# Optimization experiments

Measured on AMD Instinct MI355X. Metric: run time of the kernel, lower is better.

The kernel has to match this reference:

```python
import jax, jax.numpy as jnp
import numpy as np
from jax import lax

B, H, W = 512, 128, 128
ARCH = [1, 4096, 4096, 4096, 4096]
CONV_THRESH = 0.0
GRAPH_THRESH = 0.8
EMBED_DIM = 1


def setup_inputs() -> dict:
    key = jax.random.key(0)
    ks = jax.random.split(key, 16)
    inp = {
        "x": jax.random.normal(ks[0], (B, 1, H, W), dtype=jnp.float32),
        "conv_w": jax.random.normal(ks[1], (1, 1, 2, 2), dtype=jnp.float32) * 0.5,
        "conv_b": jax.random.normal(ks[2], (1,), dtype=jnp.float32) * 0.1,
        "rotation": jax.random.normal(ks[3], (EMBED_DIM, EMBED_DIM), dtype=jnp.float32),
        "entangle": jax.random.normal(ks[4], (EMBED_DIM, EMBED_DIM), dtype=jnp.float32),
    }
    # Linear params, torch convention W: [out_f, in_f]
    for i, (fi, fo) in enumerate(zip(ARCH[:-1], ARCH[1:])):
        inp[f"W{i+1}"] = jax.random.normal(ks[5 + 2 * i], (fo, fi), dtype=jnp.float32) / np.sqrt(fi)
        inp[f"b{i+1}"] = jax.random.normal(ks[6 + 2 * i], (fo,), dtype=jnp.float32) * 0.01
    return inp


def _forward(x, conv_w, conv_b, rotation, entangle, W1, b1, W2, b2, W3, b3, W4, b4):
    # ConvFilter: 2x2 valid conv, sigmoid(logits - thresh), mean over C,H,W -> [B]
    logits = lax.conv_general_dilated(
        x, conv_w, window_strides=(1, 1), padding="VALID",
        dimension_numbers=("NCHW", "OIHW", "NCHW"))
    logits = logits + conv_b.reshape(1, -1, 1, 1)
    conv_out = jax.nn.sigmoid(logits - CONV_THRESH).mean(axis=(1, 2, 3))  # [B]
    conv_vec = conv_out[:, None]  # [B, 1] -> embed_dim forced to 1

    # ClassicalSelfAttention (embed_dim = 1)
    q = conv_vec @ rotation                      # [B, 1]
    k = conv_vec @ entangle                      # [B, 1]
    scores = jax.nn.softmax((q @ k.T) / np.sqrt(EMBED_DIM).astype(np.float32), axis=-1)  # [B, B]
    attn_out = scores @ conv_vec                 # [B, 1]

    # tanh MLP stack
    out = attn_out
    acts = []
    for Wl, bl in ((W1, b1), (W2, b2), (W3, b3), (W4, b4)):
        out = jnp.tanh(out @ Wl.T + bl)          # [B, out_f]
        acts.append(out)

    # Vectorized fidelity adjacency over equal-shaped layer activations:
    # normalized Gram matrix squared, thresholded (replaces the O(L^2)
    # Python loop with .item() syncs in the source).
    S = jnp.stack([a.reshape(-1) for a in acts])                  # [L, B*4096]
    S_hat = S / (jnp.linalg.norm(S, axis=1, keepdims=True) + 1e-12)
    fid = (S_hat @ S_hat.T) ** 2                                   # [L, L]
    L = len(acts)
    weights = jnp.where(fid >= GRAPH_THRESH, 1.0, 0.0) * (1.0 - jnp.eye(L, dtype=fid.dtype))
    return out, weights


def reference(x, conv_w, conv_b, rotation, entangle, W1, b1, W2, b2, W3, b3, W4, b4):
    return _forward(x, conv_w, conv_b, rotation, entangle, W1, b1, W2, b2, W3, b3, W4, b4)
```

## Files before the change

### kernel.cpp

```cpp
#include <hip/hip_runtime.h>
#include <cmath>


#define NEL (512 * 4096)

typedef float  floatx4 __attribute__((ext_vector_type(4)));
typedef _Float16 halfx8 __attribute__((ext_vector_type(8)));

__global__ __launch_bounds__(256) void conv_mean_kernel(
    const float* __restrict__ x, const float* __restrict__ cw,
    const float* __restrict__ cb, float* __restrict__ c_out)
{
  __shared__ float sbuf[4];
  const int b = blockIdx.x;
  const float w00 = cw[0], w01 = cw[1], w10 = cw[2], w11 = cw[3];
  const float bias = cb[0];
  const float* xb = x + (size_t)b * 128 * 128;
  float acc = 0.f;
  for (int idx = threadIdx.x; idx < 127 * 127; idx += 256) {
    int i = idx / 127;
    int j = idx - i * 127;
    const float* p = xb + i * 128 + j;
    float v = w00 * p[0] + w01 * p[1] + w10 * p[128] + w11 * p[129] + bias;
    acc += 1.0f / (1.0f + __expf(-v));
  }
  #pragma unroll
  for (int off = 32; off > 0; off >>= 1) acc += __shfl_down(acc, off, 64);
  const int lane = threadIdx.x & 63, wv = threadIdx.x >> 6;
  if (lane == 0) sbuf[wv] = acc;
  __syncthreads();
  if (threadIdx.x == 0)
    c_out[b] = (sbuf[0] + sbuf[1] + sbuf[2] + sbuf[3]) * (1.0f / 16129.0f);
}

__global__ __launch_bounds__(64) void attn_kernel(
    const float* __restrict__ c, const float* __restrict__ rot,
    const float* __restrict__ ent, float* __restrict__ attn)
{
  const int i = blockIdx.x;
  const int lane = threadIdx.x;
  const float t = rot[0] * ent[0] * c[i];
  float vals[8], cj[8];
  float mx = -1e30f;
  #pragma unroll
  for (int u = 0; u < 8; ++u) {
    float cv = c[lane + u * 64];
    cj[u] = cv;
    vals[u] = t * cv;
    mx = fmaxf(mx, vals[u]);
  }
  #pragma unroll
  for (int off = 32; off > 0; off >>= 1) mx = fmaxf(mx, __shfl_down(mx, off, 64));
  mx = __shfl(mx, 0, 64);
  float se = 0.f, sw = 0.f;
  #pragma unroll
  for (int u = 0; u < 8; ++u) {
    float e = __expf(vals[u] - mx);
    se += e;
    sw += e * cj[u];
  }
  #pragma unroll
  for (int off = 32; off > 0; off >>= 1) {
    se += __shfl_down(se, off, 64);
    sw += __shfl_down(sw, off, 64);
  }
  if (lane == 0) attn[i] = sw / se;
}

__global__ __launch_bounds__(256) void layer1_kernel(
    const float* __restrict__ attn, const float* __restrict__ W1,
    const float* __restrict__ b1, float* __restrict__ act1)
{
  const int o = blockIdx.x * 256 + threadIdx.x;
  const int i = blockIdx.y;
  act1[(size_t)i * 4096 + o] = tanhf(attn[i] * W1[o] + b1[o]);
}

#define BM 128
#define BN 128
#define BK 32
#define LDK 40

template<bool FUSE>
__global__ __launch_bounds__(256) void gemm_tanh_kernel(
    const float* __restrict__ A, const float* __restrict__ W,
    const float* __restrict__ bias, float* __restrict__ C)
{
  __shared__ _Float16 As[BM][LDK];
  __shared__ _Float16 Ws[BN][LDK];
  const int K = 4096, N = 4096;
  const int tid  = threadIdx.x;
  const int lane = tid & 63;
  const int wave = tid >> 6;
  const int wm = (wave >> 1) * 64;
  const int wn = (wave & 1) * 64;
  const int q  = lane >> 4;
  const int ml = lane & 15;
  const int tileM = blockIdx.y * BM;
  const int tileN = blockIdx.x * BN;
  const int Kslice = K / gridDim.z;
  const int kbeg = blockIdx.z * Kslice;
  const int kend = kbeg + Kslice;
  float* Cb = FUSE ? C : C + (size_t)blockIdx.z * NEL;

  floatx4 acc[4][4] = {};

  const int r0  = tid >> 2;
  const int cc0 = (tid & 3) << 3;

  float4 pa[4], pw[4];
  auto load_tile = [&](int k0) {
    #pragma unroll
    for (int u = 0; u < 2; ++u) {
      const float* ap = A + (size_t)(tileM + r0 + u * 64) * K + k0 + cc0;
      pa[2 * u]     = *reinterpret_cast<const float4*>(ap);
      pa[2 * u + 1] = *reinterpret_cast<const float4*>(ap + 4);
      const float* wp = W + (size_t)(tileN + r0 + u * 64) * K + k0 + cc0;
      pw[2 * u]     = *reinterpret_cast<const float4*>(wp);
      pw[2 * u + 1] = *reinterpret_cast<const float4*>(wp + 4);
    }
  };
  auto store_tile = [&]() {
    #pragma unroll
    for (int u = 0; u < 2; ++u) {
      halfx8 ha = { (_Float16)pa[2*u].x, (_Float16)pa[2*u].y,
                    (_Float16)pa[2*u].z, (_Float16)pa[2*u].w,
                    (_Float16)pa[2*u+1].x, (_Float16)pa[2*u+1].y,
                    (_Float16)pa[2*u+1].z, (_Float16)pa[2*u+1].w };
      *reinterpret_cast<halfx8*>(&As[r0 + u * 64][cc0]) = ha;
      halfx8 hw = { (_Float16)pw[2*u].x, (_Float16)pw[2*u].y,
                    (_Float16)pw[2*u].z, (_Float16)pw[2*u].w,
                    (_Float16)pw[2*u+1].x, (_Float16)pw[2*u+1].y,
                    (_Float16)pw[2*u+1].z, (_Float16)pw[2*u+1].w };
      *reinterpret_cast<halfx8*>(&Ws[r0 + u * 64][cc0]) = hw;
    }
  };

  load_tile(kbeg);
  for (int k0 = kbeg; k0 < kend; k0 += BK) {
    __syncthreads();
    store_tile();
    __syncthreads();
    if (k0 + BK < kend) load_tile(k0 + BK);

    halfx8 af[4], bf[4];
    #pragma unroll
    for (int i = 0; i < 4; ++i)
      af[i] = *reinterpret_cast<const halfx8*>(&As[wm + i * 16 + ml][q * 8]);
    #pragma unroll
    for (int j = 0; j < 4; ++j)
      bf[j] = *reinterpret_cast<const halfx8*>(&Ws[wn + j * 16 + ml][q * 8]);

    #pragma unroll
    for (int i = 0; i < 4; ++i)
      #pragma unroll
      for (int j = 0; j < 4; ++j)
        acc[i][j] = __builtin_amdgcn_mfma_f32_16x16x32_f16(af[i], bf[j], acc[i][j], 0, 0, 0);
  }

  #pragma unroll
  for (int i = 0; i < 4; ++i) {
    const int row0 = tileM + wm + i * 16 + q * 4;
    #pragma unroll
    for (int j = 0; j < 4; ++j) {
      const int col = tileN + wn + j * 16 + ml;
      if (FUSE) {
        const float bv = bias[col];
        #pragma unroll
        for (int r = 0; r < 4; ++r)
          Cb[(size_t)(row0 + r) * N + col] = tanhf(acc[i][j][r] + bv);
      } else {
        #pragma unroll
        for (int r = 0; r < 4; ++r)
          Cb[(size_t)(row0 + r) * N + col] = acc[i][j][r];
      }
    }
  }
}

template<int S>
__global__ __launch_bounds__(256) void combine_tanh_kernel(
    const float* __restrict__ part, const float* __restrict__ bias,
    float* __restrict__ outp)
{
  const int i4 = blockIdx.x * 256 + threadIdx.x;
  const floatx4* p4 = (const floatx4*)part;
  floatx4 s = p4[i4];
  #pragma unroll
  for (int z = 1; z < S; ++z) s += p4[(size_t)z * (NEL / 4) + i4];
  const floatx4 bv = ((const floatx4*)bias)[i4 & 1023];
  floatx4 o;
  #pragma unroll
  for (int r = 0; r < 4; ++r) o[r] = tanhf(s[r] + bv[r]);
  ((floatx4*)outp)[i4] = o;
}

__global__ __launch_bounds__(256) void fid_dots_kernel(
    const float* __restrict__ a1, const float* __restrict__ a2,
    const float* __restrict__ a3, const float* __restrict__ a4,
    float* __restrict__ D)
{
  __shared__ float sred[4][10];
  float s[10] = {0, 0, 0, 0, 0, 0, 0, 0, 0, 0};
  const int n4 = NEL / 4;
  const int stride = gridDim.x * blockDim.x;
  const floatx4* p1 = (const floatx4*)a1;
  const floatx4* p2 = (const floatx4*)a2;
  const floatx4* p3 = (const floatx4*)a3;
  const floatx4* p4 = (const floatx4*)a4;
  for (int i = blockIdx.x * 256 + threadIdx.x; i < n4; i += stride) {
    floatx4 v1 = p1[i], v2 = p2[i], v3 = p3[i], v4 = p4[i];
    #pragma unroll
    for (int r = 0; r < 4; ++r) {
      s[0] += v1[r] * v1[r]; s[1] += v1[r] * v2[r]; s[2] += v1[r] * v3[r];
      s[3] += v1[r] * v4[r]; s[4] += v2[r] * v2[r]; s[5] += v2[r] * v3[r];
      s[6] += v2[r] * v4[r]; s[7] += v3[r] * v3[r]; s[8] += v3[r] * v4[r];
      s[9] += v4[r] * v4[r];
    }
  }
  const int lane = threadIdx.x & 63, wv = threadIdx.x >> 6;
  #pragma unroll
  for (int p = 0; p < 10; ++p) {
    float v = s[p];
    #pragma unroll
    for (int off = 32; off > 0; off >>= 1) v += __shfl_down(v, off, 64);
    if (lane == 0) sred[wv][p] = v;
  }
  __syncthreads();
  if (threadIdx.x < 10) {
    float v = sred[0][threadIdx.x] + sred[1][threadIdx.x] +
              sred[2][threadIdx.x] + sred[3][threadIdx.x];
    atomicAdd(&D[threadIdx.x * 16], v);
  }
}

__global__ void finalize_kernel(const float* __restrict__ D, float* __restrict__ wout)
{
  const int i = threadIdx.x;
  if (i >= 16) return;
  const int p = i >> 2, qq = i & 3;
  const int a = p < qq ? p : qq;
  const int b = p < qq ? qq : p;
  const int base[4] = {0, 4, 7, 9};
  const float dpq = D[(base[a] + (b - a)) * 16];
  const float npv = sqrtf(D[base[p] * 16]) + 1e-12f;
  const float nqv = sqrtf(D[base[qq] * 16]) + 1e-12f;
  const float ch = dpq / (npv * nqv);
  const float fid = ch * ch;
  wout[i] = (fid >= 0.8f && p != qq) ? 1.0f : 0.0f;
}

extern "C" void kernel_launch(void* const* d_in, const int* in_sizes, int n_in,
                              void* d_out, int out_size, void* d_ws, size_t ws_size,
                              hipStream_t stream)
{
  const float* x   = (const float*)d_in[0];
  const float* cw  = (const float*)d_in[1];
  const float* cb  = (const float*)d_in[2];
  const float* rot = (const float*)d_in[3];
  const float* ent = (const float*)d_in[4];
  const float* W1  = (const float*)d_in[5];
  const float* b1  = (const float*)d_in[6];
  const float* W2  = (const float*)d_in[7];
  const float* b2  = (const float*)d_in[8];
  const float* W3  = (const float*)d_in[9];
  const float* b3  = (const float*)d_in[10];
  const float* W4  = (const float*)d_in[11];
  const float* b4  = (const float*)d_in[12];
  float* out = (float*)d_out;

  char*  ws    = (char*)d_ws;
  float* c_buf = (float*)(ws + 0);
  float* attn  = (float*)(ws + 2048);
  float* D     = (float*)(ws + 4096);
  float* act1  = (float*)(ws + 8192);
  float* act2  = act1 + NEL;
  float* act3  = act2 + NEL;
  float* part  = act3 + NEL;
  float* wout  = out + NEL;

  const size_t base_need = 8192 + (size_t)3 * NEL * 4;
  const bool sk8 = ws_size >= base_need + (size_t)8 * NEL * 4;
  const bool sk4 = ws_size >= base_need + (size_t)4 * NEL * 4;

  hipMemsetAsync(D, 0, 10 * 16 * sizeof(float), stream);
  conv_mean_kernel<<<512, 256, 0, stream>>>(x, cw, cb, c_buf);
  attn_kernel<<<512, 64, 0, stream>>>(c_buf, rot, ent, attn);
  layer1_kernel<<<dim3(16, 512), 256, 0, stream>>>(attn, W1, b1, act1);

  const int cgrid = NEL / 4 / 256;
  if (sk8) {
    dim3 g(4096 / BN, 512 / BM, 8);
    gemm_tanh_kernel<false><<<g, 256, 0, stream>>>(act1, W2, nullptr, part);
    combine_tanh_kernel<8><<<cgrid, 256, 0, stream>>>(part, b2, act2);
    gemm_tanh_kernel<false><<<g, 256, 0, stream>>>(act2, W3, nullptr, part);
    combine_tanh_kernel<8><<<cgrid, 256, 0, stream>>>(part, b3, act3);
    gemm_tanh_kernel<false><<<g, 256, 0, stream>>>(act3, W4, nullptr, part);
    combine_tanh_kernel<8><<<cgrid, 256, 0, stream>>>(part, b4, out);
  } else if (sk4) {
    dim3 g(4096 / BN, 512 / BM, 4);
    gemm_tanh_kernel<false><<<g, 256, 0, stream>>>(act1, W2, nullptr, part);
    combine_tanh_kernel<4><<<cgrid, 256, 0, stream>>>(part, b2, act2);
    gemm_tanh_kernel<false><<<g, 256, 0, stream>>>(act2, W3, nullptr, part);
    combine_tanh_kernel<4><<<cgrid, 256, 0, stream>>>(part, b3, act3);
    gemm_tanh_kernel<false><<<g, 256, 0, stream>>>(act3, W4, nullptr, part);
    combine_tanh_kernel<4><<<cgrid, 256, 0, stream>>>(part, b4, out);
  } else {
    dim3 g(4096 / BN, 512 / BM, 1);
    gemm_tanh_kernel<true><<<g, 256, 0, stream>>>(act1, W2, b2, act2);
    gemm_tanh_kernel<true><<<g, 256, 0, stream>>>(act2, W3, b3, act3);
    gemm_tanh_kernel<true><<<g, 256, 0, stream>>>(act3, W4, b4, out);
  }

  fid_dots_kernel<<<256, 256, 0, stream>>>(act1, act2, act3, out, D);
  finalize_kernel<<<1, 64, 0, stream>>>(D, wout);
}
```

Before: 456.2 us.

## Double-buffer GEMM LDS tiles and vectorize conv loads

The GEMM kernel now uses two LDS buffers, so the next tile is written into the idle buffer after the MFMAs. This cuts the loop to one barrier per K step and lets the global loads overlap the matrix math. Launch bounds now request 4 blocks per SIMD, which may raise register pressure or cause spills. The conv kernel now reads each row with float4 loads and computes four outputs per thread instead of indexing each output with a division.

```diff
diff --git a/kernel.cpp b/kernel.cpp
--- a/kernel.cpp
+++ b/kernel.cpp
@@ -17,12 +17,24 @@
   const float bias = cb[0];
   const float* xb = x + (size_t)b * 128 * 128;
   float acc = 0.f;
-  for (int idx = threadIdx.x; idx < 127 * 127; idx += 256) {
-    int i = idx / 127;
-    int j = idx - i * 127;
-    const float* p = xb + i * 128 + j;
-    float v = w00 * p[0] + w01 * p[1] + w10 * p[128] + w11 * p[129] + bias;
-    acc += 1.0f / (1.0f + __expf(-v));
+  for (int t = threadIdx.x; t < 127 * 32; t += 256) {
+    const int i  = t >> 5;
+    const int j0 = (t & 31) << 2;
+    const float* pr0 = xb + i * 128 + j0;
+    const float* pr1 = pr0 + 128;
+    const float4 a4 = *reinterpret_cast<const float4*>(pr0);
+    const float  a5 = pr0[4];
+    const float4 b4 = *reinterpret_cast<const float4*>(pr1);
+    const float  b5 = pr1[4];
+    const float a[5] = {a4.x, a4.y, a4.z, a4.w, a5};
+    const float bb[5] = {b4.x, b4.y, b4.z, b4.w, b5};
+    #pragma unroll
+    for (int m = 0; m < 4; ++m) {
+      if (j0 + m < 127) {
+        float v = w00 * a[m] + w01 * a[m + 1] + w10 * bb[m] + w11 * bb[m + 1] + bias;
+        acc += 1.0f / (1.0f + __expf(-v));
+      }
+    }
   }
   #pragma unroll
   for (int off = 32; off > 0; off >>= 1) acc += __shfl_down(acc, off, 64);
@@ -82,12 +94,12 @@
 #define LDK 40
 
 template<bool FUSE>
-__global__ __launch_bounds__(256) void gemm_tanh_kernel(
+__global__ __launch_bounds__(256, 4) void gemm_tanh_kernel(
     const float* __restrict__ A, const float* __restrict__ W,
     const float* __restrict__ bias, float* __restrict__ C)
 {
-  __shared__ _Float16 As[BM][LDK];
-  __shared__ _Float16 Ws[BN][LDK];
+  __shared__ _Float16 As[2][BM][LDK];
+  __shared__ _Float16 Ws[2][BN][LDK];
   const int K = 4096, N = 4096;
   const int tid  = threadIdx.x;
   const int lane = tid & 63;
@@ -120,42 +132,47 @@
       pw[2 * u + 1] = *reinterpret_cast<const float4*>(wp + 4);
     }
   };
-  auto store_tile = [&]() {
+  auto store_tile = [&](int buf) {
     #pragma unroll
     for (int u = 0; u < 2; ++u) {
       halfx8 ha = { (_Float16)pa[2*u].x, (_Float16)pa[2*u].y,
                     (_Float16)pa[2*u].z, (_Float16)pa[2*u].w,
                     (_Float16)pa[2*u+1].x, (_Float16)pa[2*u+1].y,
                     (_Float16)pa[2*u+1].z, (_Float16)pa[2*u+1].w };
-      *reinterpret_cast<halfx8*>(&As[r0 + u * 64][cc0]) = ha;
+      *reinterpret_cast<halfx8*>(&As[buf][r0 + u * 64][cc0]) = ha;
       halfx8 hw = { (_Float16)pw[2*u].x, (_Float16)pw[2*u].y,
                     (_Float16)pw[2*u].z, (_Float16)pw[2*u].w,
                     (_Float16)pw[2*u+1].x, (_Float16)pw[2*u+1].y,
                     (_Float16)pw[2*u+1].z, (_Float16)pw[2*u+1].w };
-      *reinterpret_cast<halfx8*>(&Ws[r0 + u * 64][cc0]) = hw;
+      *reinterpret_cast<halfx8*>(&Ws[buf][r0 + u * 64][cc0]) = hw;
     }
   };
 
   load_tile(kbeg);
+  store_tile(0);
+  int cur = 0;
+
   for (int k0 = kbeg; k0 < kend; k0 += BK) {
+    const bool more = (k0 + BK < kend);
+    if (more) load_tile(k0 + BK);
     __syncthreads();
-    store_tile();
-    __syncthreads();
-    if (k0 + BK < kend) load_tile(k0 + BK);
 
     halfx8 af[4], bf[4];
     #pragma unroll
     for (int i = 0; i < 4; ++i)
-      af[i] = *reinterpret_cast<const halfx8*>(&As[wm + i * 16 + ml][q * 8]);
+      af[i] = *reinterpret_cast<const halfx8*>(&As[cur][wm + i * 16 + ml][q * 8]);
     #pragma unroll
     for (int j = 0; j < 4; ++j)
-      bf[j] = *reinterpret_cast<const halfx8*>(&Ws[wn + j * 16 + ml][q * 8]);
+      bf[j] = *reinterpret_cast<const halfx8*>(&Ws[cur][wn + j * 16 + ml][q * 8]);
 
     #pragma unroll
     for (int i = 0; i < 4; ++i)
       #pragma unroll
       for (int j = 0; j < 4; ++j)
         acc[i][j] = __builtin_amdgcn_mfma_f32_16x16x32_f16(af[i], bf[j], acc[i][j], 0, 0, 0);
+
+    if (more) store_tile(cur ^ 1);
+    cur ^= 1;
   }
 
   #pragma unroll
```

Result: faster. 425.3 us (-6.8%).
